# Optimization experiments

Hardware: AMD Instinct MI355X
Metric: run time of the kernel (lower is better)

## Reference

```python
import jax, jax.numpy as jnp
import numpy as np

NUM_HEADS = 12
HEAD_DIM = 64  # d_out // num_heads = 768 // 12


def setup_inputs() -> dict:
    key = jax.random.key(0)
    k1, k2 = jax.random.split(key)
    x = jax.random.normal(k1, (2, 2048, 768), dtype=jnp.float32)
    # torch Linear weight: [d_out, d_in], y = x @ W.T
    Wq = jax.random.normal(k2, (768, 768), dtype=jnp.float32) * 0.02
    return {"x": x, "Wq": Wq}


def reference(x, Wq):
    b, n, d_in = x.shape
    H, hd = NUM_HEADS, HEAD_DIM
    d_out = H * hd
    # NOTE: the original module uses Wq for queries, keys AND values.
    qkv = x @ Wq.T                                   # [b, n, d_out]
    h = qkv.reshape(b, n, H, hd).transpose(0, 2, 1, 3)  # [b, H, n, hd]
    scores = jnp.einsum('bhqd,bhkd->bhqk', h, h)      # [b, H, n, n]
    causal = jnp.triu(jnp.ones((n, n), dtype=bool), k=1)
    scores = jnp.where(causal, -jnp.inf, scores)
    attn = jax.nn.softmax(scores / jnp.sqrt(jnp.float32(hd)), axis=-1)
    ctx = jnp.einsum('bhqk,bhkd->bhqd', attn, h)      # [b, H, n, hd]
    # faithful to source: transpose(-2,-1) -> [b, H, hd, n], then view(b, n, d_out)
    ctx = ctx.transpose(0, 1, 3, 2)
    return ctx.reshape(b, n, d_out)
```

## Files before the change

### kernel.cpp

```cpp
#include <hip/hip_runtime.h>
#include <math.h>

typedef __attribute__((ext_vector_type(8))) short  short8;
typedef __attribute__((ext_vector_type(4))) float  floatx4;

#define MFMA16(a, b, c) __builtin_amdgcn_mfma_f32_16x16x32_bf16(a, b, c, 0, 0, 0)

constexpr int NSEQ = 2048;
constexpr int DIN  = 768;
constexpr int NH   = 12;
constexpr float QSCALE = 0.18033688011112042f;

constexpr int PK = 72;

__device__ __forceinline__ ushort f2bf(float f) {
    unsigned u = __float_as_uint(f);
    u += 0x7FFF + ((u >> 16) & 1);
    return (ushort)(u >> 16);
}
__device__ __forceinline__ float bf2f(ushort u) {
    return __uint_as_float(((unsigned)u) << 16);
}
__device__ __forceinline__ unsigned cvt_pk_bf16(float lo, float hi) {
    unsigned r;
    asm("v_cvt_pk_bf16_f32 %0, %1, %2" : "=v"(r) : "v"(lo), "v"(hi));
    return r;
}
__device__ __forceinline__ short8 pk8(float4 a, float4 b) {
    union { unsigned u[4]; short8 s; } r;
    r.u[0] = cvt_pk_bf16(a.x, a.y);
    r.u[1] = cvt_pk_bf16(a.z, a.w);
    r.u[2] = cvt_pk_bf16(b.x, b.y);
    r.u[3] = cvt_pk_bf16(b.z, b.w);
    return r.s;
}
__device__ __forceinline__ void bar_lds() {
    asm volatile("s_waitcnt lgkmcnt(0)" ::: "memory");
    __builtin_amdgcn_s_barrier();
}

__global__ __launch_bounds__(256, 3)
void qkv_mfma(const float* __restrict__ x, const float* __restrict__ Wq,
              ushort* __restrict__ h)
{
    __shared__ ushort As[2][64 * PK];
    __shared__ ushort Bs[2][64 * PK];

    const int tid  = threadIdx.x;
    const int w    = tid >> 6;
    const int lane = tid & 63;
    const int m    = lane & 15;
    const int quad = lane >> 4;
    const int r0   = blockIdx.x * 64;
    const int c0   = blockIdx.y * 64;
    const int mrow0 = (w & 1) * 32;
    const int ncol0 = (w >> 1) * 32;

    const int srow = tid >> 3;
    const int scol = (tid & 7) * 8;

    floatx4 C[2][2] = {};
    float4 arf[2][2], brf[2][2];

    #pragma unroll
    for (int i = 0; i < 2; ++i) {
        const float* ax = x  + (size_t)(r0 + srow + i * 32) * DIN + scol;
        const float* bx = Wq + (size_t)(c0 + srow + i * 32) * DIN + scol;
        arf[i][0] = ((const float4*)ax)[0]; arf[i][1] = ((const float4*)ax)[1];
        brf[i][0] = ((const float4*)bx)[0]; brf[i][1] = ((const float4*)bx)[1];
    }
    #pragma unroll
    for (int i = 0; i < 2; ++i) {
        *(short8*)&As[0][(srow + i * 32) * PK + scol] = pk8(arf[i][0], arf[i][1]);
        *(short8*)&Bs[0][(srow + i * 32) * PK + scol] = pk8(brf[i][0], brf[i][1]);
    }
    #pragma unroll
    for (int i = 0; i < 2; ++i) {
        const float* ax = x  + (size_t)(r0 + srow + i * 32) * DIN + 64 + scol;
        const float* bx = Wq + (size_t)(c0 + srow + i * 32) * DIN + 64 + scol;
        arf[i][0] = ((const float4*)ax)[0]; arf[i][1] = ((const float4*)ax)[1];
        brf[i][0] = ((const float4*)bx)[0]; brf[i][1] = ((const float4*)bx)[1];
    }
    bar_lds();

    for (int kk = 0; kk < 12; ++kk) {
        const int cur = kk & 1;

        #pragma unroll
        for (int kt2 = 0; kt2 < 2; ++kt2) {
            short8 a0 = *(const short8*)&As[cur][(mrow0 + m)      * PK + kt2 * 32 + quad * 8];
            short8 a1 = *(const short8*)&As[cur][(mrow0 + 16 + m) * PK + kt2 * 32 + quad * 8];
            short8 b0 = *(const short8*)&Bs[cur][(ncol0 + m)      * PK + kt2 * 32 + quad * 8];
            short8 b1 = *(const short8*)&Bs[cur][(ncol0 + 16 + m) * PK + kt2 * 32 + quad * 8];
            C[0][0] = MFMA16(a0, b0, C[0][0]);
            C[0][1] = MFMA16(a0, b1, C[0][1]);
            C[1][0] = MFMA16(a1, b0, C[1][0]);
            C[1][1] = MFMA16(a1, b1, C[1][1]);
        }

        if (kk + 1 < 12) {
            const int nxt = cur ^ 1;
            #pragma unroll
            for (int i = 0; i < 2; ++i) {
                *(short8*)&As[nxt][(srow + i * 32) * PK + scol] = pk8(arf[i][0], arf[i][1]);
                *(short8*)&Bs[nxt][(srow + i * 32) * PK + scol] = pk8(brf[i][0], brf[i][1]);
            }
            if (kk + 2 < 12) {
                const int k0 = (kk + 2) * 64;
                #pragma unroll
                for (int i = 0; i < 2; ++i) {
                    const float* ax = x  + (size_t)(r0 + srow + i * 32) * DIN + k0 + scol;
                    const float* bx = Wq + (size_t)(c0 + srow + i * 32) * DIN + k0 + scol;
                    arf[i][0] = ((const float4*)ax)[0]; arf[i][1] = ((const float4*)ax)[1];
                    brf[i][0] = ((const float4*)bx)[0]; brf[i][1] = ((const float4*)bx)[1];
                }
            }
            bar_lds();
        }
    }

    #pragma unroll
    for (int mt = 0; mt < 2; ++mt)
        #pragma unroll
        for (int nt = 0; nt < 2; ++nt) {
            int cg = c0 + ncol0 + nt * 16 + m;
            int head = cg >> 6, d = cg & 63;
            #pragma unroll
            for (int r = 0; r < 4; ++r) {
                int rg = r0 + mrow0 + mt * 16 + quad * 4 + r;
                int b = rg >> 11, q = rg & 2047;
                h[((size_t)(b * NH + head) * NSEQ + q) * 64 + d] = f2bf(C[mt][nt][r]);
            }
        }
}

__global__ __launch_bounds__(256, 3)
void attn_mfma(const ushort* __restrict__ h, float* __restrict__ out)
{
    __shared__ ushort Ks[2][64 * PK];
    __shared__ ushort Vt[2][64 * PK];
    __shared__ ushort Ps[2][16 * PK];

    const int tid  = threadIdx.x;
    const int w    = tid >> 6;
    const int lane = tid & 63;
    const int m    = lane & 15;
    const int quad = lane >> 4;
    const int qsub = w & 1;
    const int khalf= w >> 1;

    const int p  = blockIdx.x;
    const int bh = blockIdx.y;
    const ushort* __restrict__ Hh = h + (size_t)bh * NSEQ * 64;
    ushort* Psw = Ps[qsub];

    const int kr2  = (tid & 31) * 2;
    const int part = tid >> 5;
    const int db   = part * 8;

    float* Om = (float*)&Ks[0][0];
    float* Lm = Om + 2 * 64 * 17;

    #pragma unroll 1
    for (int half = 0; half < 2; ++half) {
        if (half) bar_lds();

        const int qt  = half ? p : (63 - p);
        const int q0  = qt * 32;
        const int wq  = q0 + qsub * 16;
        const int nkt = (qt >> 1) + 1;

        short8 qa[2];
        #pragma unroll
        for (int kt2 = 0; kt2 < 2; ++kt2) {
            short8 raw = *(const short8*)(Hh + (size_t)(wq + m) * 64 + kt2 * 32 + quad * 8);
            #pragma unroll
            for (int j = 0; j < 8; ++j)
                qa[kt2][j] = (short)f2bf(bf2f((ushort)raw[j]) * QSCALE);
        }

        floatx4 O[4] = {};
        float lacc = 0.0f;

        short8 pre0, pre1;
        {
            const ushort* src = Hh + (size_t)kr2 * 64 + db;
            pre0 = *(const short8*)src;
            pre1 = *(const short8*)(src + 64);
        }
        {
            *(short8*)&Ks[0][kr2       * PK + db] = pre0;
            *(short8*)&Ks[0][(kr2 + 1) * PK + db] = pre1;
            union { short8 v; ushort u[8]; } ua, ub;
            ua.v = pre0; ub.v = pre1;
            #pragma unroll
            for (int i = 0; i < 8; ++i)
                *(unsigned*)&Vt[0][(db + i) * PK + kr2] =
                    (unsigned)ua.u[i] | ((unsigned)ub.u[i] << 16);
        }
        if (nkt > 1) {
            const ushort* src = Hh + (size_t)(64 + kr2) * 64 + db;
            pre0 = *(const short8*)src;
            pre1 = *(const short8*)(src + 64);
        }
        bar_lds();

        for (int kt = 0; kt < nkt; ++kt) {
            const int cur = kt & 1;

            floatx4 S[2] = {};
            #pragma unroll
            for (int kt2 = 0; kt2 < 2; ++kt2)
                #pragma unroll
                for (int mt2 = 0; mt2 < 2; ++mt2) {
                    short8 ka = *(const short8*)
                        &Ks[cur][(khalf * 32 + mt2 * 16 + m) * PK + kt2 * 32 + quad * 8];
                    S[mt2] = MFMA16(ka, qa[kt2], S[mt2]);
                }

            const int lim  = wq + m - kt * 64;
            const bool diag = (kt == nkt - 1);
            #pragma unroll
            for (int mt2 = 0; mt2 < 2; ++mt2) {
                const int kb = (khalf * 2 + mt2) * 16 + quad * 4;
                float p0, p1, p2, p3;
                if (diag) {
                    p0 = (kb + 0 <= lim) ? exp2f(S[mt2][0]) : 0.0f;
                    p1 = (kb + 1 <= lim) ? exp2f(S[mt2][1]) : 0.0f;
                    p2 = (kb + 2 <= lim) ? exp2f(S[mt2][2]) : 0.0f;
                    p3 = (kb + 3 <= lim) ? exp2f(S[mt2][3]) : 0.0f;
                } else {
                    p0 = exp2f(S[mt2][0]);
                    p1 = exp2f(S[mt2][1]);
                    p2 = exp2f(S[mt2][2]);
                    p3 = exp2f(S[mt2][3]);
                }
                lacc += (p0 + p1) + (p2 + p3);
                uint2 pw;
                pw.x = cvt_pk_bf16(p0, p1);
                pw.y = cvt_pk_bf16(p2, p3);
                *(uint2*)&Psw[m * PK + kb] = pw;
            }

            short8 pb = *(const short8*)&Psw[m * PK + khalf * 32 + quad * 8];
            #pragma unroll
            for (int mt = 0; mt < 4; ++mt) {
                short8 va = *(const short8*)
                    &Vt[cur][(mt * 16 + m) * PK + khalf * 32 + quad * 8];
                O[mt] = MFMA16(va, pb, O[mt]);
            }

            if (kt + 1 < nkt) {
                const int nxt = cur ^ 1;
                *(short8*)&Ks[nxt][kr2       * PK + db] = pre0;
                *(short8*)&Ks[nxt][(kr2 + 1) * PK + db] = pre1;
                union { short8 v; ushort u[8]; } ua, ub;
                ua.v = pre0; ub.v = pre1;
                #pragma unroll
                for (int i = 0; i < 8; ++i)
                    *(unsigned*)&Vt[nxt][(db + i) * PK + kr2] =
                        (unsigned)ua.u[i] | ((unsigned)ub.u[i] << 16);
                if (kt + 2 < nkt) {
                    const ushort* src = Hh + (size_t)((kt + 2) * 64 + kr2) * 64 + db;
                    pre0 = *(const short8*)src;
                    pre1 = *(const short8*)(src + 64);
                }
            }
            bar_lds();
        }

        lacc += __shfl_xor(lacc, 16);
        lacc += __shfl_xor(lacc, 32);
        if (khalf == 1) {
            #pragma unroll
            for (int mt = 0; mt < 4; ++mt)
                #pragma unroll
                for (int r = 0; r < 4; ++r) {
                    int d = mt * 16 + quad * 4 + r;
                    Om[(qsub * 64 + d) * 17 + m] = O[mt][r];
                }
            if (quad == 0) Lm[qsub * 16 + m] = lacc;
        }
        bar_lds();
        if (khalf == 0) {
            float linv = 1.0f / (lacc + Lm[qsub * 16 + m]);
            #pragma unroll
            for (int mt = 0; mt < 4; ++mt)
                #pragma unroll
                for (int r = 0; r < 4; ++r) {
                    int d = mt * 16 + quad * 4 + r;
                    float v = O[mt][r] + Om[(qsub * 64 + d) * 17 + m];
                    out[((size_t)bh * 64 + d) * NSEQ + q0 + qsub * 16 + m] = v * linv;
                }
        }
    }
}

extern "C" void kernel_launch(void* const* d_in, const int* in_sizes, int n_in,
                              void* d_out, int out_size, void* d_ws, size_t ws_size,
                              hipStream_t stream)
{
    (void)in_sizes; (void)n_in; (void)out_size; (void)ws_size;
    const float* x  = (const float*)d_in[0];
    const float* Wq = (const float*)d_in[1];
    float* out = (float*)d_out;

    ushort* hb = (ushort*)d_ws;

    qkv_mfma<<<dim3(64, 12), dim3(256), 0, stream>>>(x, Wq, hb);
    attn_mfma<<<dim3(32, 24), dim3(256), 0, stream>>>(hb, out);
}
```

Before: 114.9 us.

## Split paired q-tiles into separate blocks and single-buffer K/V for occupancy

Each block now handles one 32-row query tile instead of a heavy/light pair, with the grid doubled to 64x24 and tile order flipped per head group to balance causal work. K/V LDS staging drops from double to single buffering, which roughly halves shared memory per block and raises the launch-bounds occupancy target from 3 to 6 blocks. In exchange, each iteration needs two barriers and the global-to-LDS store is no longer overlapped with compute inside the block, so overlap has to come from more resident blocks. Per-block load balance also becomes uneven.

```diff
diff --git a/kernel.cpp b/kernel.cpp
--- a/kernel.cpp
+++ b/kernel.cpp
@@ -134,12 +134,12 @@
         }
 }
 
-__global__ __launch_bounds__(256, 3)
+__global__ __launch_bounds__(256, 6)
 void attn_mfma(const ushort* __restrict__ h, float* __restrict__ out)
 {
-    __shared__ ushort Ks[2][64 * PK];
-    __shared__ ushort Vt[2][64 * PK];
-    __shared__ ushort Ps[2][16 * PK];
+    __shared__ ushort Ks[64 * PK];
+    __shared__ ushort Vt[64 * PK];
+    __shared__ ushort Ps[2 * 16 * PK];
 
     const int tid  = threadIdx.x;
     const int w    = tid >> 6;
@@ -149,150 +149,126 @@
     const int qsub = w & 1;
     const int khalf= w >> 1;
 
-    const int p  = blockIdx.x;
+    const int xi = blockIdx.x;
     const int bh = blockIdx.y;
+    const int qt = ((bh >> 2) & 1) ? xi : (63 - xi);
+    const int q0 = qt * 32;
+    const int wq = q0 + qsub * 16;
+    const int nkt = (qt >> 1) + 1;
     const ushort* __restrict__ Hh = h + (size_t)bh * NSEQ * 64;
-    ushort* Psw = Ps[qsub];
+    ushort* Psw = Ps + qsub * 16 * PK;
 
     const int kr2  = (tid & 31) * 2;
     const int part = tid >> 5;
     const int db   = part * 8;
 
-    float* Om = (float*)&Ks[0][0];
-    float* Lm = Om + 2 * 64 * 17;
-
-    #pragma unroll 1
-    for (int half = 0; half < 2; ++half) {
-        if (half) bar_lds();
-
-        const int qt  = half ? p : (63 - p);
-        const int q0  = qt * 32;
-        const int wq  = q0 + qsub * 16;
-        const int nkt = (qt >> 1) + 1;
-
-        short8 qa[2];
-        #pragma unroll
-        for (int kt2 = 0; kt2 < 2; ++kt2) {
-            short8 raw = *(const short8*)(Hh + (size_t)(wq + m) * 64 + kt2 * 32 + quad * 8);
-            #pragma unroll
-            for (int j = 0; j < 8; ++j)
-                qa[kt2][j] = (short)f2bf(bf2f((ushort)raw[j]) * QSCALE);
-        }
-
-        floatx4 O[4] = {};
-        float lacc = 0.0f;
-
-        short8 pre0, pre1;
-        {
-            const ushort* src = Hh + (size_t)kr2 * 64 + db;
+    short8 qa[2];
+    #pragma unroll
+    for (int kt2 = 0; kt2 < 2; ++kt2) {
+        short8 raw = *(const short8*)(Hh + (size_t)(wq + m) * 64 + kt2 * 32 + quad * 8);
+        #pragma unroll
+        for (int j = 0; j < 8; ++j)
+            qa[kt2][j] = (short)f2bf(bf2f((ushort)raw[j]) * QSCALE);
+    }
+
+    floatx4 O[4] = {};
+    float lacc = 0.0f;
+
+    short8 pre0, pre1;
+    {
+        const ushort* src = Hh + (size_t)kr2 * 64 + db;
+        pre0 = *(const short8*)src;
+        pre1 = *(const short8*)(src + 64);
+    }
+
+    for (int kt = 0; kt < nkt; ++kt) {
+        bar_lds();
+
+        *(short8*)&Ks[kr2       * PK + db] = pre0;
+        *(short8*)&Ks[(kr2 + 1) * PK + db] = pre1;
+        union { short8 v; ushort u[8]; } ua, ub;
+        ua.v = pre0; ub.v = pre1;
+        #pragma unroll
+        for (int i = 0; i < 8; ++i)
+            *(unsigned*)&Vt[(db + i) * PK + kr2] =
+                (unsigned)ua.u[i] | ((unsigned)ub.u[i] << 16);
+        if (kt + 1 < nkt) {
+            const ushort* src = Hh + (size_t)((kt + 1) * 64 + kr2) * 64 + db;
             pre0 = *(const short8*)src;
             pre1 = *(const short8*)(src + 64);
         }
-        {
-            *(short8*)&Ks[0][kr2       * PK + db] = pre0;
-            *(short8*)&Ks[0][(kr2 + 1) * PK + db] = pre1;
-            union { short8 v; ushort u[8]; } ua, ub;
-            ua.v = pre0; ub.v = pre1;
-            #pragma unroll
-            for (int i = 0; i < 8; ++i)
-                *(unsigned*)&Vt[0][(db + i) * PK + kr2] =
-                    (unsigned)ua.u[i] | ((unsigned)ub.u[i] << 16);
-        }
-        if (nkt > 1) {
-            const ushort* src = Hh + (size_t)(64 + kr2) * 64 + db;
-            pre0 = *(const short8*)src;
-            pre1 = *(const short8*)(src + 64);
-        }
         bar_lds();
 
-        for (int kt = 0; kt < nkt; ++kt) {
-            const int cur = kt & 1;
-
-            floatx4 S[2] = {};
-            #pragma unroll
-            for (int kt2 = 0; kt2 < 2; ++kt2)
-                #pragma unroll
-                for (int mt2 = 0; mt2 < 2; ++mt2) {
-                    short8 ka = *(const short8*)
-                        &Ks[cur][(khalf * 32 + mt2 * 16 + m) * PK + kt2 * 32 + quad * 8];
-                    S[mt2] = MFMA16(ka, qa[kt2], S[mt2]);
-                }
-
-            const int lim  = wq + m - kt * 64;
-            const bool diag = (kt == nkt - 1);
+        floatx4 S[2] = {};
+        #pragma unroll
+        for (int kt2 = 0; kt2 < 2; ++kt2)
             #pragma unroll
             for (int mt2 = 0; mt2 < 2; ++mt2) {
-                const int kb = (khalf * 2 + mt2) * 16 + quad * 4;
-                float p0, p1, p2, p3;
-                if (diag) {
-                    p0 = (kb + 0 <= lim) ? exp2f(S[mt2][0]) : 0.0f;
-                    p1 = (kb + 1 <= lim) ? exp2f(S[mt2][1]) : 0.0f;
-                    p2 = (kb + 2 <= lim) ? exp2f(S[mt2][2]) : 0.0f;
-                    p3 = (kb + 3 <= lim) ? exp2f(S[mt2][3]) : 0.0f;
-                } else {
-                    p0 = exp2f(S[mt2][0]);
-                    p1 = exp2f(S[mt2][1]);
-                    p2 = exp2f(S[mt2][2]);
-                    p3 = exp2f(S[mt2][3]);
-                }
-                lacc += (p0 + p1) + (p2 + p3);
-                uint2 pw;
-                pw.x = cvt_pk_bf16(p0, p1);
-                pw.y = cvt_pk_bf16(p2, p3);
-                *(uint2*)&Psw[m * PK + kb] = pw;
-            }
-
-            short8 pb = *(const short8*)&Psw[m * PK + khalf * 32 + quad * 8];
-            #pragma unroll
-            for (int mt = 0; mt < 4; ++mt) {
-                short8 va = *(const short8*)
-                    &Vt[cur][(mt * 16 + m) * PK + khalf * 32 + quad * 8];
-                O[mt] = MFMA16(va, pb, O[mt]);
-            }
-
-            if (kt + 1 < nkt) {
-                const int nxt = cur ^ 1;
-                *(short8*)&Ks[nxt][kr2       * PK + db] = pre0;
-                *(short8*)&Ks[nxt][(kr2 + 1) * PK + db] = pre1;
-                union { short8 v; ushort u[8]; } ua, ub;
-                ua.v = pre0; ub.v = pre1;
-                #pragma unroll
-                for (int i = 0; i < 8; ++i)
-                    *(unsigned*)&Vt[nxt][(db + i) * PK + kr2] =
-                        (unsigned)ua.u[i] | ((unsigned)ub.u[i] << 16);
-                if (kt + 2 < nkt) {
-                    const ushort* src = Hh + (size_t)((kt + 2) * 64 + kr2) * 64 + db;
-                    pre0 = *(const short8*)src;
-                    pre1 = *(const short8*)(src + 64);
-                }
-            }
-            bar_lds();
-        }
-
-        lacc += __shfl_xor(lacc, 16);
-        lacc += __shfl_xor(lacc, 32);
-        if (khalf == 1) {
-            #pragma unroll
-            for (int mt = 0; mt < 4; ++mt)
-                #pragma unroll
-                for (int r = 0; r < 4; ++r) {
-                    int d = mt * 16 + quad * 4 + r;
-                    Om[(qsub * 64 + d) * 17 + m] = O[mt][r];
-                }
-            if (quad == 0) Lm[qsub * 16 + m] = lacc;
-        }
-        bar_lds();
-        if (khalf == 0) {
-            float linv = 1.0f / (lacc + Lm[qsub * 16 + m]);
-            #pragma unroll
-            for (int mt = 0; mt < 4; ++mt)
-                #pragma unroll
-                for (int r = 0; r < 4; ++r) {
-                    int d = mt * 16 + quad * 4 + r;
-                    float v = O[mt][r] + Om[(qsub * 64 + d) * 17 + m];
-                    out[((size_t)bh * 64 + d) * NSEQ + q0 + qsub * 16 + m] = v * linv;
-                }
-        }
+                short8 ka = *(const short8*)
+                    &Ks[(khalf * 32 + mt2 * 16 + m) * PK + kt2 * 32 + quad * 8];
+                S[mt2] = MFMA16(ka, qa[kt2], S[mt2]);
+            }
+
+        const int lim  = wq + m - kt * 64;
+        const bool diag = (kt == nkt - 1);
+        #pragma unroll
+        for (int mt2 = 0; mt2 < 2; ++mt2) {
+            const int kb = (khalf * 2 + mt2) * 16 + quad * 4;
+            float p0, p1, p2, p3;
+            if (diag) {
+                p0 = (kb + 0 <= lim) ? exp2f(S[mt2][0]) : 0.0f;
+                p1 = (kb + 1 <= lim) ? exp2f(S[mt2][1]) : 0.0f;
+                p2 = (kb + 2 <= lim) ? exp2f(S[mt2][2]) : 0.0f;
+                p3 = (kb + 3 <= lim) ? exp2f(S[mt2][3]) : 0.0f;
+            } else {
+                p0 = exp2f(S[mt2][0]);
+                p1 = exp2f(S[mt2][1]);
+                p2 = exp2f(S[mt2][2]);
+                p3 = exp2f(S[mt2][3]);
+            }
+            lacc += (p0 + p1) + (p2 + p3);
+            uint2 pw;
+            pw.x = cvt_pk_bf16(p0, p1);
+            pw.y = cvt_pk_bf16(p2, p3);
+            *(uint2*)&Psw[m * PK + kb] = pw;
+        }
+
+        short8 pb = *(const short8*)&Psw[m * PK + khalf * 32 + quad * 8];
+        #pragma unroll
+        for (int mt = 0; mt < 4; ++mt) {
+            short8 va = *(const short8*)
+                &Vt[(mt * 16 + m) * PK + khalf * 32 + quad * 8];
+            O[mt] = MFMA16(va, pb, O[mt]);
+        }
+    }
+
+    lacc += __shfl_xor(lacc, 16);
+    lacc += __shfl_xor(lacc, 32);
+
+    float* Om = (float*)&Ks[0];
+    float* Lm = Om + 2 * 64 * 17;
+    bar_lds();
+    if (khalf == 1) {
+        #pragma unroll
+        for (int mt = 0; mt < 4; ++mt)
+            #pragma unroll
+            for (int r = 0; r < 4; ++r) {
+                int d = mt * 16 + quad * 4 + r;
+                Om[(qsub * 64 + d) * 17 + m] = O[mt][r];
+            }
+        if (quad == 0) Lm[qsub * 16 + m] = lacc;
+    }
+    bar_lds();
+    if (khalf == 0) {
+        float linv = 1.0f / (lacc + Lm[qsub * 16 + m]);
+        #pragma unroll
+        for (int mt = 0; mt < 4; ++mt)
+            #pragma unroll
+            for (int r = 0; r < 4; ++r) {
+                int d = mt * 16 + quad * 4 + r;
+                float v = O[mt][r] + Om[(qsub * 64 + d) * 17 + m];
+                out[((size_t)bh * 64 + d) * NSEQ + q0 + qsub * 16 + m] = v * linv;
+            }
     }
 }
 
@@ -308,5 +284,5 @@
     ushort* hb = (ushort*)d_ws;
 
     qkv_mfma<<<dim3(64, 12), dim3(256), 0, stream>>>(x, Wq, hb);
-    attn_mfma<<<dim3(32, 24), dim3(256), 0, stream>>>(hb, out);
-}
+    attn_mfma<<<dim3(64, 24), dim3(256), 0, stream>>>(hb, out);
+}
```

Result: no change. 116.9 us (+1.7%).
